# Kernel tuning notes

Hardware: AMD Instinct MI355X
Metric: run time of the kernel (lower is better)

Reference implementation:

```python
import jax, jax.numpy as jnp
import numpy as np

KERNEL = 301  # sliding max window length (odd -> same-size output)
TOPK = 2


def setup_inputs() -> dict:
    key = jax.random.key(0)
    xcorr = jax.random.normal(key, (32, 3, 64, 8192), dtype=jnp.float32)
    return {"xcorr": xcorr, "nlag": 4096}


def reference(xcorr, nlag):
    # xcorr: [nb, nc, nx, nt]
    x = jnp.abs(xcorr)  # vabs=True
    pad = KERNEL // 2
    # sliding-window max over time axis (== F.max_pool2d((1,K), stride 1, pad K//2))
    smax = jax.lax.reduce_window(
        x,
        -jnp.inf,
        jax.lax.max,
        window_dimensions=(1, 1, 1, KERNEL),
        window_strides=(1, 1, 1, 1),
        padding=[(0, 0), (0, 0), (0, 0), (pad, pad)],
    )
    # keep only local maxima, zero elsewhere (x * (smax == x).float())
    scores = jnp.where(smax == x, x, jnp.zeros((), x.dtype))
    topk_score, topk_idx = jax.lax.top_k(scores, TOPK)  # [nb, nc, nx, TOPK]
    return topk_score, topk_idx
```

## Files before the change

kernel.cpp:

```cpp
#include <hip/hip_runtime.h>
#include <stdint.h>


#define NT 8192
#define RADIUS 150
#define NTHREADS 256
#define NSEG (NT / 32)
#define MPAD (NSEG + 16)

__global__ __launch_bounds__(256) void detect_peaks_kernel(
    const float* __restrict__ x, float* __restrict__ out, int nrows)
{
    const int row = blockIdx.x;
    const int tid = threadIdx.x;

    __shared__ float m[MPAD];
    __shared__ unsigned long long wred[8];

    const float* grow = x + (size_t)row * NT;
    const float4* g4 = (const float4*)grow;

    if (tid < MPAD - NSEG) m[NSEG + tid] = 0.0f;

    float4 vv[8];
#pragma unroll
    for (int it = 0; it < 8; ++it) vv[it] = g4[it * 256 + tid];

    unsigned int cmask = 0u;
#pragma unroll
    for (int it = 0; it < 8; ++it) {
        const float4 v = vv[it];
        const float ax = fabsf(v.x), ay = fabsf(v.y);
        const float az = fabsf(v.z), aw = fabsf(v.w);
        const float cm4 = fmaxf(fmaxf(ax, ay), fmaxf(az, aw));
        float cm = fmaxf(cm4, __shfl_xor(cm4, 1));
        cm = fmaxf(cm, __shfl_xor(cm, 2));
        cm = fmaxf(cm, __shfl_xor(cm, 4));
        const int c = it * 256 + tid;
        if ((tid & 7) == 0) m[c >> 3] = cm;
        cmask |= (ax == cm ? 1u : 0u) << (it * 4 + 0);
        cmask |= (ay == cm ? 1u : 0u) << (it * 4 + 1);
        cmask |= (az == cm ? 1u : 0u) << (it * 4 + 2);
        cmask |= (aw == cm ? 1u : 0u) << (it * 4 + 3);
    }
    __syncthreads();

    unsigned long long k1 = 0ull, k2 = 0ull;
    unsigned int mask = cmask;

    while (__ballot(mask != 0u) != 0ull) {
        const bool active = (mask != 0u);
        int i = 0;
        if (active) { i = __builtin_ctz(mask); mask &= (mask - 1u); }
        const int t = ((i >> 2) << 10) + (tid << 2) + (i & 3);
        if (active) {
            const int l = max(t - RADIUS, 0);
            const int r = min(t + RADIUS, NT - 1);
            const int il = l >> 5, ir = r >> 5;
            const float val = m[t >> 5];
            const int len = ir - il - 1;
            const float* mp = &m[il + 1];
            float iv[9];
#pragma unroll
            for (int j = 0; j < 9; ++j) iv[j] = mp[j];
            float im = 0.0f;
#pragma unroll
            for (int j = 0; j < 9; ++j) im = fmaxf(im, (j < len) ? iv[j] : 0.0f);
            if (!(im > val)) {
                float em = 0.0f;
                const int hb0 = l >> 2;
                const int hbN = il * 8 + 8;
#pragma unroll
                for (int j = 0; j < 8; ++j) {
                    const int b = hb0 + j;
                    const float4 q = g4[b];
                    float bm;
                    if (j == 0) {
                        bm = (4 * b + 0 >= l) ? fabsf(q.x) : 0.0f;
                        bm = fmaxf(bm, (4 * b + 1 >= l) ? fabsf(q.y) : 0.0f);
                        bm = fmaxf(bm, (4 * b + 2 >= l) ? fabsf(q.z) : 0.0f);
                        bm = fmaxf(bm, fabsf(q.w));
                    } else {
                        bm = fmaxf(fmaxf(fabsf(q.x), fabsf(q.y)),
                                   fmaxf(fabsf(q.z), fabsf(q.w)));
                    }
                    em = fmaxf(em, (b < hbN) ? bm : 0.0f);
                }
                const int tb0 = ir * 8;
#pragma unroll
                for (int j = 0; j < 8; ++j) {
                    const int b = tb0 + j;
                    const float4 q = g4[b];
                    float bm;
                    bm = (4 * b + 0 <= r) ? fabsf(q.x) : 0.0f;
                    bm = fmaxf(bm, (4 * b + 1 <= r) ? fabsf(q.y) : 0.0f);
                    bm = fmaxf(bm, (4 * b + 2 <= r) ? fabsf(q.z) : 0.0f);
                    bm = fmaxf(bm, (4 * b + 3 <= r) ? fabsf(q.w) : 0.0f);
                    em = fmaxf(em, bm);
                }
                if (!(em > val)) {
                    const unsigned long long key =
                        ((unsigned long long)__float_as_uint(val) << 32) |
                        (unsigned)(NT - 1 - t);
                    if (key > k1) { k2 = k1; k1 = key; }
                    else if (key > k2) { k2 = key; }
                }
            }
        }
    }

#pragma unroll
    for (int off = 32; off >= 1; off >>= 1) {
        unsigned long long o1 = __shfl_down(k1, off);
        unsigned long long o2 = __shfl_down(k2, off);
        unsigned long long hi = (k1 > o1) ? k1 : o1;
        unsigned long long lo = (k1 > o1) ? o1 : k1;
        unsigned long long s2 = (k2 > o2) ? k2 : o2;
        k1 = hi;
        k2 = (lo > s2) ? lo : s2;
    }
    const int wave = tid >> 6;
    if ((tid & 63) == 0) { wred[wave * 2] = k1; wred[wave * 2 + 1] = k2; }
    __syncthreads();

    if (tid == 0) {
        unsigned long long a1 = wred[0], a2 = wred[1];
        for (int w = 1; w < 4; ++w) {
            unsigned long long o1 = wred[w * 2], o2 = wred[w * 2 + 1];
            unsigned long long hi = (a1 > o1) ? a1 : o1;
            unsigned long long lo = (a1 > o1) ? o1 : a1;
            unsigned long long s2 = (a2 > o2) ? a2 : o2;
            a1 = hi;
            a2 = (lo > s2) ? lo : s2;
        }
        float s1v, s2v; int i1, i2;
        if (a1 == 0ull) { s1v = 0.0f; i1 = 0; }
        else {
            s1v = __uint_as_float((unsigned)(a1 >> 32));
            i1 = (NT - 1) - (int)(a1 & 0xffffffffull);
        }
        if (a2 == 0ull) {
            s2v = 0.0f;
            i2 = (i1 == 0) ? 1 : 0;
        } else {
            s2v = __uint_as_float((unsigned)(a2 >> 32));
            i2 = (NT - 1) - (int)(a2 & 0xffffffffull);
        }
        out[row * 2 + 0] = s1v;
        out[row * 2 + 1] = s2v;
        float* oi = out + (size_t)nrows * 2;
        oi[row * 2 + 0] = (float)i1;
        oi[row * 2 + 1] = (float)i2;
    }
}

extern "C" void kernel_launch(void* const* d_in, const int* in_sizes, int n_in,
                              void* d_out, int out_size, void* d_ws, size_t ws_size,
                              hipStream_t stream) {
    const float* x = (const float*)d_in[0];
    float* out = (float*)d_out;
    const int nrows = in_sizes[0] / NT;
    detect_peaks_kernel<<<nrows, NTHREADS, 0, stream>>>(x, out, nrows);
}
```

Before: 285.8 us.

## Split peak detection into segment-max pass and per-segment candidate pass

Splits the kernel in two. The first pass computes per-32-element segment maxima and candidate bitmasks and writes them to workspace. The second pass maps one thread to one segment, loops over that segment's candidates, and runs the window verification and top-2 reduction. This is meant to balance the candidate loop across lanes and shrink register pressure in each kernel, at the cost of an extra launch, a workspace round trip, and the x row being read from global memory a second time.

Result: slower. 300.8 us (+5.2%).

```diff
diff --git a/kernel.cpp b/kernel.cpp
--- a/kernel.cpp
+++ b/kernel.cpp
@@ -4,29 +4,21 @@
 
 #define NT 8192
 #define RADIUS 150
-#define NTHREADS 256
-#define NSEG (NT / 32)
-#define MPAD (NSEG + 16)
+#define NSEG 256
 
-__global__ __launch_bounds__(256) void detect_peaks_kernel(
-    const float* __restrict__ x, float* __restrict__ out, int nrows)
+__global__ __launch_bounds__(256, 8) void seg_pass(
+    const float* __restrict__ x, float2* __restrict__ ws)
 {
     const int row = blockIdx.x;
     const int tid = threadIdx.x;
-
-    __shared__ float m[MPAD];
-    __shared__ unsigned long long wred[8];
-
-    const float* grow = x + (size_t)row * NT;
-    const float4* g4 = (const float4*)grow;
-
-    if (tid < MPAD - NSEG) m[NSEG + tid] = 0.0f;
+    const float4* g4 = (const float4*)(x + (size_t)row * NT);
+    float2* wrow = ws + (size_t)row * NSEG;
 
     float4 vv[8];
 #pragma unroll
     for (int it = 0; it < 8; ++it) vv[it] = g4[it * 256 + tid];
 
-    unsigned int cmask = 0u;
+    const int sh = (tid & 7) * 4;
 #pragma unroll
     for (int it = 0; it < 8; ++it) {
         const float4 v = vv[it];
@@ -36,77 +28,100 @@
         float cm = fmaxf(cm4, __shfl_xor(cm4, 1));
         cm = fmaxf(cm, __shfl_xor(cm, 2));
         cm = fmaxf(cm, __shfl_xor(cm, 4));
-        const int c = it * 256 + tid;
-        if ((tid & 7) == 0) m[c >> 3] = cm;
-        cmask |= (ax == cm ? 1u : 0u) << (it * 4 + 0);
-        cmask |= (ay == cm ? 1u : 0u) << (it * 4 + 1);
-        cmask |= (az == cm ? 1u : 0u) << (it * 4 + 2);
-        cmask |= (aw == cm ? 1u : 0u) << (it * 4 + 3);
+        unsigned msk = ((ax == cm ? 1u : 0u) |
+                        (ay == cm ? 2u : 0u) |
+                        (az == cm ? 4u : 0u) |
+                        (aw == cm ? 8u : 0u)) << sh;
+        msk |= __shfl_xor((int)msk, 1);
+        msk |= __shfl_xor((int)msk, 2);
+        msk |= __shfl_xor((int)msk, 4);
+        if ((tid & 7) == 0) {
+            const int seg = (it * 256 + tid) >> 3;
+            wrow[seg] = make_float2(cm, __uint_as_float(msk));
+        }
     }
+}
+
+__global__ __launch_bounds__(256) void peaks_pass(
+    const float* __restrict__ x, const float2* __restrict__ ws,
+    float* __restrict__ out, int nrows)
+{
+    const int row = blockIdx.x;
+    const int s = threadIdx.x;
+
+    __shared__ float mm[8 + NSEG + 16];
+    __shared__ unsigned long long wred[8];
+    float* const mmp = mm + 8;
+
+    const float2 w = ws[(size_t)row * NSEG + s];
+    const float sval = w.x;
+    unsigned msk = __float_as_uint(w.y);
+
+    if (s < 8) mm[s] = 0.0f;
+    if (s < 16) mm[8 + NSEG + s] = 0.0f;
+    mmp[s] = sval;
     __syncthreads();
 
+    const float4* g4 = (const float4*)(x + (size_t)row * NT);
     unsigned long long k1 = 0ull, k2 = 0ull;
-    unsigned int mask = cmask;
 
-    while (__ballot(mask != 0u) != 0ull) {
-        const bool active = (mask != 0u);
-        int i = 0;
-        if (active) { i = __builtin_ctz(mask); mask &= (mask - 1u); }
-        const int t = ((i >> 2) << 10) + (tid << 2) + (i & 3);
-        if (active) {
-            const int l = max(t - RADIUS, 0);
-            const int r = min(t + RADIUS, NT - 1);
-            const int il = l >> 5, ir = r >> 5;
-            const float val = m[t >> 5];
-            const int len = ir - il - 1;
-            const float* mp = &m[il + 1];
-            float iv[9];
+    while (msk) {
+        const int b = __builtin_ctz(msk); msk &= (msk - 1u);
+        const int t = (s << 5) + b;
+        const float val = sval;
+        const int l = max(t - RADIUS, 0);
+        const int r = min(t + RADIUS, NT - 1);
+        const int il = l >> 5, ir = r >> 5;
+        const int len = ir - il - 1;
+        const float* mp = &mmp[il + 1];
+        float iv[9];
 #pragma unroll
-            for (int j = 0; j < 9; ++j) iv[j] = mp[j];
-            float im = 0.0f;
+        for (int j = 0; j < 9; ++j) iv[j] = mp[j];
+        float im = 0.0f;
 #pragma unroll
-            for (int j = 0; j < 9; ++j) im = fmaxf(im, (j < len) ? iv[j] : 0.0f);
-            if (!(im > val)) {
-                float em = 0.0f;
-                const int hb0 = l >> 2;
-                const int hbN = il * 8 + 8;
+        for (int j = 0; j < 9; ++j) im = fmaxf(im, (j < len) ? iv[j] : 0.0f);
+        if (im > val) continue;
+        float em = 0.0f;
+        {
+            const int hb0 = l >> 2;
+            const int hbN = il * 8 + 8;
 #pragma unroll
-                for (int j = 0; j < 8; ++j) {
-                    const int b = hb0 + j;
-                    const float4 q = g4[b];
-                    float bm;
-                    if (j == 0) {
-                        bm = (4 * b + 0 >= l) ? fabsf(q.x) : 0.0f;
-                        bm = fmaxf(bm, (4 * b + 1 >= l) ? fabsf(q.y) : 0.0f);
-                        bm = fmaxf(bm, (4 * b + 2 >= l) ? fabsf(q.z) : 0.0f);
-                        bm = fmaxf(bm, fabsf(q.w));
-                    } else {
-                        bm = fmaxf(fmaxf(fabsf(q.x), fabsf(q.y)),
-                                   fmaxf(fabsf(q.z), fabsf(q.w)));
-                    }
-                    em = fmaxf(em, (b < hbN) ? bm : 0.0f);
+            for (int j = 0; j < 8; ++j) {
+                const int bb = hb0 + j;
+                const float4 q = g4[bb];
+                float bm;
+                if (j == 0) {
+                    bm = (4 * bb + 0 >= l) ? fabsf(q.x) : 0.0f;
+                    bm = fmaxf(bm, (4 * bb + 1 >= l) ? fabsf(q.y) : 0.0f);
+                    bm = fmaxf(bm, (4 * bb + 2 >= l) ? fabsf(q.z) : 0.0f);
+                    bm = fmaxf(bm, fabsf(q.w));
+                } else {
+                    bm = fmaxf(fmaxf(fabsf(q.x), fabsf(q.y)),
+                               fmaxf(fabsf(q.z), fabsf(q.w)));
                 }
-                const int tb0 = ir * 8;
-#pragma unroll
-                for (int j = 0; j < 8; ++j) {
-                    const int b = tb0 + j;
-                    const float4 q = g4[b];
-                    float bm;
-                    bm = (4 * b + 0 <= r) ? fabsf(q.x) : 0.0f;
-                    bm = fmaxf(bm, (4 * b + 1 <= r) ? fabsf(q.y) : 0.0f);
-                    bm = fmaxf(bm, (4 * b + 2 <= r) ? fabsf(q.z) : 0.0f);
-                    bm = fmaxf(bm, (4 * b + 3 <= r) ? fabsf(q.w) : 0.0f);
-                    em = fmaxf(em, bm);
-                }
-                if (!(em > val)) {
-                    const unsigned long long key =
-                        ((unsigned long long)__float_as_uint(val) << 32) |
-                        (unsigned)(NT - 1 - t);
-                    if (key > k1) { k2 = k1; k1 = key; }
-                    else if (key > k2) { k2 = key; }
-                }
+                em = fmaxf(em, (bb < hbN) ? bm : 0.0f);
             }
         }
+        {
+            const int tb0 = ir * 8;
+#pragma unroll
+            for (int j = 0; j < 8; ++j) {
+                const int bb = tb0 + j;
+                const float4 q = g4[bb];
+                float bm;
+                bm = (4 * bb + 0 <= r) ? fabsf(q.x) : 0.0f;
+                bm = fmaxf(bm, (4 * bb + 1 <= r) ? fabsf(q.y) : 0.0f);
+                bm = fmaxf(bm, (4 * bb + 2 <= r) ? fabsf(q.z) : 0.0f);
+                bm = fmaxf(bm, (4 * bb + 3 <= r) ? fabsf(q.w) : 0.0f);
+                em = fmaxf(em, bm);
+            }
+        }
+        if (em > val) continue;
+        const unsigned long long key =
+            ((unsigned long long)__float_as_uint(val) << 32) |
+            (unsigned)(NT - 1 - t);
+        if (key > k1) { k2 = k1; k1 = key; }
+        else if (key > k2) { k2 = key; }
     }
 
 #pragma unroll
@@ -119,14 +134,14 @@
         k1 = hi;
         k2 = (lo > s2) ? lo : s2;
     }
-    const int wave = tid >> 6;
-    if ((tid & 63) == 0) { wred[wave * 2] = k1; wred[wave * 2 + 1] = k2; }
+    const int wave = s >> 6;
+    if ((s & 63) == 0) { wred[wave * 2] = k1; wred[wave * 2 + 1] = k2; }
     __syncthreads();
 
-    if (tid == 0) {
+    if (s == 0) {
         unsigned long long a1 = wred[0], a2 = wred[1];
-        for (int w = 1; w < 4; ++w) {
-            unsigned long long o1 = wred[w * 2], o2 = wred[w * 2 + 1];
+        for (int wv = 1; wv < 4; ++wv) {
+            unsigned long long o1 = wred[wv * 2], o2 = wred[wv * 2 + 1];
             unsigned long long hi = (a1 > o1) ? a1 : o1;
             unsigned long long lo = (a1 > o1) ? o1 : a1;
             unsigned long long s2 = (a2 > o2) ? a2 : o2;
@@ -160,5 +175,7 @@
     const float* x = (const float*)d_in[0];
     float* out = (float*)d_out;
     const int nrows = in_sizes[0] / NT;
-    detect_peaks_kernel<<<nrows, NTHREADS, 0, stream>>>(x, out, nrows);
+    float2* ws = (float2*)d_ws;
+    seg_pass<<<nrows, 256, 0, stream>>>(x, ws);
+    peaks_pass<<<nrows, 256, 0, stream>>>(x, ws, out, nrows);
 }
```
